# Performance work log

Hardware: AMD Instinct MI355X
Metric: run time of the kernel (lower is better)

The kernel has to match this reference:

```python
import jax, jax.numpy as jnp
import numpy as np

B, D, L, H, W, T = 256, 512, 32, 14, 14, 8


def _lin(x, w, b=None):
    y = x @ w.T
    return y if b is None else y + b


def _conv1x1(x, w, b):  # x: [B,C,H,W], w: [O,C], b: [O]
    return jnp.einsum('oc,bchw->bohw', w, x) + b[None, :, None, None]


def setup_inputs() -> dict:
    key = jax.random.key(0)
    ks = jax.random.split(key, 24)
    s = 0.02
    inp = {
        'c': jax.random.normal(ks[0], (B, D), jnp.float32),
        'm': jax.random.normal(ks[1], (B, D), jnp.float32),
        'k': jax.random.normal(ks[2], (B, D, H, W), jnp.float32),
        'q': jax.random.normal(ks[3], (B, D), jnp.float32),
        'cw': jax.random.normal(ks[4], (B, L, D), jnp.float32),
        'mask': jax.random.randint(ks[5], (B, L), 0, 2, jnp.int32),
        'cs': jax.random.normal(ks[6], (T, B, D), jnp.float32),
        'ms': jax.random.normal(ks[7], (T, B, D), jnp.float32),
        # ControlUnit params
        'Wcq': jax.random.normal(ks[8], (D, 2 * D), jnp.float32) * s,
        'bcq': jnp.zeros((D,), jnp.float32),
        'Wca': jax.random.normal(ks[9], (1, D), jnp.float32) * s,
        'bca': jnp.zeros((1,), jnp.float32),
        # ReadUnit params
        'Wm_r': jax.random.normal(ks[10], (D, D), jnp.float32) * s,
        'bm_r': jnp.zeros((D,), jnp.float32),
        'Wk': jax.random.normal(ks[11], (D, D), jnp.float32) * s,
        'bk': jnp.zeros((D,), jnp.float32),
        'WI': jax.random.normal(ks[12], (D, 2 * D), jnp.float32) * s,
        'bI': jnp.zeros((D,), jnp.float32),
        'Wra': jax.random.normal(ks[13], (D, D), jnp.float32) * s,
        'bra': jnp.zeros((D,), jnp.float32),
        # WriteUnit params
        'Wm_w': jax.random.normal(ks[14], (D, 2 * D), jnp.float32) * s,
        'bm_w': jnp.zeros((D,), jnp.float32),
        'Wsa': jax.random.normal(ks[15], (1, D), jnp.float32) * s,
        'bsa': jnp.zeros((1,), jnp.float32),
        'Wm2': jax.random.normal(ks[16], (D, D), jnp.float32) * s,
        'bm2': jnp.zeros((D,), jnp.float32),
        'Wc': jax.random.normal(ks[17], (1, D), jnp.float32) * s,
        'bc': jnp.ones((1,), jnp.float32),  # linear_c.bias.data.fill_(1)
        'Ws': jax.random.normal(ks[18], (D, D), jnp.float32) * s,
    }
    return inp


def reference(c, m, k, q, cw, mask, cs, ms,
              Wcq, bcq, Wca, bca,
              Wm_r, bm_r, Wk, bk, WI, bI, Wra, bra,
              Wm_w, bm_w, Wsa, bsa, Wm2, bm2, Wc, bc, Ws):
    # ---- ControlUnit ----
    cq = _lin(jnp.concatenate([c, q], axis=1), Wcq, bcq)          # [B,D]
    ca = _lin(cq[:, None, :] * cw, Wca, bca)                      # [B,L,1]
    ca = jnp.where(mask[:, :, None] > 0, ca, -jnp.inf)            # mask padding
    cv = jax.nn.softmax(ca, axis=1)                               # [B,L,1]
    c_new = jnp.sum(cv * cw, axis=1)                              # [B,D]

    # ---- ReadUnit ----
    mI = _lin(m, Wm_r, bm_r)                                      # [B,D]
    I = mI[:, :, None, None] * _conv1x1(k, Wk, bk)                # [B,D,H,W]
    I_ = _conv1x1(jnp.concatenate([I, k], axis=1), WI, bI)        # [B,D,H,W]
    ra = _conv1x1(I_ * c_new[:, :, None, None], Wra, bra)         # [B,D,H,W]
    rv = jax.nn.softmax(ra, axis=1)                               # Softmax2d = over channels
    r = jnp.sum(rv * k, axis=(-1, -2))                            # [B,D]

    # ---- WriteUnit ----
    m_prev = _lin(jnp.concatenate([r, m], axis=1), Wm_w, bm_w)    # [B,D]
    m_ = _lin(m_prev, Wm2, bm2)                                   # [B,D]
    gate = jax.nn.sigmoid(_lin(c_new, Wc, bc))                    # [B,1]
    sa = jax.nn.softmax(_lin(cs * gate[None, :, :], Wsa, bsa), axis=0)  # [T,B,1]
    m_sa = jnp.sum(sa * ms, axis=0)                               # [B,D]
    m_ = m_ + m_sa @ Ws.T
    m_new = gate * m + (1.0 - gate) * m_                          # [B,D]

    return (c_new, m_new, cv, rv)
```

## Files before the change

### kernel.cpp

```cpp
#include <hip/hip_runtime.h>
#include <hip/hip_bf16.h>

#define BB 256
#define DD 512
#define LL 32
#define HWN 196
#define TT 8

typedef __hip_bfloat16 bf16;
typedef __attribute__((ext_vector_type(8))) short short8;
typedef __attribute__((ext_vector_type(4))) float f32x4;

__device__ __forceinline__ float b2f(bf16 x) { return __bfloat162float(x); }
__device__ __forceinline__ bf16 f2b(float x) { return __float2bfloat16(x); }
__device__ __forceinline__ unsigned short f2bu(float x) {
    bf16 h = __float2bfloat16(x);
    return *(unsigned short*)&h;
}
#define NEG_INF (-__builtin_huge_valf())

__global__ __launch_bounds__(256) void cvt_w_kernel(
    const float* __restrict__ src, unsigned short* __restrict__ dst, int n4)
{
    int i = blockIdx.x*256 + threadIdx.x;
    if (i < n4) {
        float4 f = ((const float4*)src)[i];
        ushort4 u;
        u.x = f2bu(f.x); u.y = f2bu(f.y); u.z = f2bu(f.z); u.w = f2bu(f.w);
        ((ushort4*)dst)[i] = u;
    }
}

__global__ __launch_bounds__(256) void small_gemm_kernel(
    const float* __restrict__ A1, int K1,
    const float* __restrict__ A2, int K2,
    const float* __restrict__ Wt, const float* __restrict__ bias,
    float* __restrict__ outf, int Dout)
{
    __shared__ float xs[1024];
    int b = blockIdx.x, tid = threadIdx.x;
    int K = K1 + K2;
    for (int i = tid; i < K; i += 256) {
        xs[i] = (i < K1) ? A1[(size_t)b*K1 + i] : A2[(size_t)b*K2 + (i - K1)];
    }
    __syncthreads();
    for (int d = tid; d < Dout; d += 256) {
        const float4* wrow = (const float4*)(Wt + (size_t)d * K);
        float acc = 0.f;
        for (int j = 0; j < K/4; ++j) {
            float4 w = wrow[j];
            acc += w.x*xs[j*4] + w.y*xs[j*4+1] + w.z*xs[j*4+2] + w.w*xs[j*4+3];
        }
        if (bias) acc += bias[d];
        outf[(size_t)b*Dout + d] = acc;
    }
}

__global__ __launch_bounds__(256) void control_kernel(
    const float* __restrict__ cq, const float* __restrict__ cw,
    const float* __restrict__ Wca, const float* __restrict__ bca,
    const int* __restrict__ mask,
    float* __restrict__ cnew_f, float* __restrict__ cv_out, float* __restrict__ cnew_out)
{
    __shared__ float u[DD];
    __shared__ float cas[LL];
    __shared__ float cvs[LL];
    int b = blockIdx.x, tid = threadIdx.x;
    for (int d = tid; d < DD; d += 256) u[d] = cq[(size_t)b*DD + d] * Wca[d];
    __syncthreads();
    int wave = tid >> 6, lane = tid & 63;
    float bca0 = bca[0];
    for (int lw = 0; lw < 8; ++lw) {
        int l = wave*8 + lw;
        const float4* w4 = (const float4*)(cw + ((size_t)(b*LL + l))*DD + lane*8);
        float4 wa = w4[0], wb = w4[1];
        const float* uu = &u[lane*8];
        float p = wa.x*uu[0] + wa.y*uu[1] + wa.z*uu[2] + wa.w*uu[3]
                + wb.x*uu[4] + wb.y*uu[5] + wb.z*uu[6] + wb.w*uu[7];
        for (int off = 32; off > 0; off >>= 1) p += __shfl_down(p, off);
        if (lane == 0) {
            float v = p + bca0;
            if (mask[b*LL + l] <= 0) v = NEG_INF;
            cas[l] = v;
        }
    }
    __syncthreads();
    if (tid < LL) {
        float mx = NEG_INF;
        for (int j = 0; j < LL; ++j) mx = fmaxf(mx, cas[j]);
        float s = 0.f;
        for (int j = 0; j < LL; ++j) s += __expf(cas[j] - mx);
        float cv = __expf(cas[tid] - mx) / s;
        cvs[tid] = cv;
        cv_out[b*LL + tid] = cv;
    }
    __syncthreads();
    for (int d = tid; d < DD; d += 256) {
        float acc = 0.f;
        for (int l = 0; l < LL; ++l) acc += cvs[l] * cw[((size_t)(b*LL + l))*DD + d];
        cnew_f[(size_t)b*DD + d] = acc;
        cnew_out[(size_t)b*DD + d] = acc;
    }
}

__device__ __forceinline__ void load4rows(const void* X, int isf32, size_t row, int n4, ushort4 r[4]) {
    if (isf32) {
        const float* p = (const float*)X + row*HWN + n4*4;
        #pragma unroll
        for (int i = 0; i < 4; ++i) {
            float4 f = *(const float4*)(p + (size_t)i*HWN);
            r[i].x = f2bu(f.x); r[i].y = f2bu(f.y); r[i].z = f2bu(f.z); r[i].w = f2bu(f.w);
        }
    } else {
        const unsigned short* p = (const unsigned short*)X + row*HWN + n4*4;
        #pragma unroll
        for (int i = 0; i < 4; ++i) r[i] = *(const ushort4*)(p + (size_t)i*HWN);
    }
}

__global__ __launch_bounds__(512) void conv_mfma_kernel(
    const void* __restrict__ X1, int x1f32, int C1,
    const void* __restrict__ X2, int x2f32,
    const unsigned short* __restrict__ Wb, int C,
    const float* __restrict__ bias, const float* __restrict__ oscale,
    unsigned short* __restrict__ Y)
{
    __shared__ __align__(16) uint2 Xs[8*212];
    int b = blockIdx.x, ot = blockIdx.y;
    int tid = threadIdx.x;
    int wave = tid >> 6, lane = tid & 63;
    int wm = wave >> 1, wn = wave & 1;
    int obase = ot*128 + wm*32;
    int n0 = wn*112;
    int ntn = wn ? 6 : 7;
    int ln = lane & 15, lq = lane >> 4;
    int C2 = C - C1;

    int n4_0 = tid % 49, kq_0 = tid / 49;
    bool st = tid < 8*49;

    f32x4 acc[2][7];
    #pragma unroll
    for (int mt = 0; mt < 2; ++mt)
        #pragma unroll
        for (int nt = 0; nt < 7; ++nt) acc[mt][nt] = (f32x4){0.f, 0.f, 0.f, 0.f};

    for (int c0 = 0; c0 < C; c0 += 32) {
        __syncthreads();
        if (st) {
            int c = c0 + kq_0*4;
            ushort4 r[4];
            if (c < C1) load4rows(X1, x1f32, (size_t)b*C1 + c, n4_0, r);
            else        load4rows(X2, x2f32, (size_t)b*C2 + (c - C1), n4_0, r);
            uint2* cell = &Xs[kq_0*212 + n4_0*4];
            *(uint4*)(cell) = make_uint4(
                (uint)r[0].x | ((uint)r[1].x << 16), (uint)r[2].x | ((uint)r[3].x << 16),
                (uint)r[0].y | ((uint)r[1].y << 16), (uint)r[2].y | ((uint)r[3].y << 16));
            *(uint4*)(cell + 2) = make_uint4(
                (uint)r[0].z | ((uint)r[1].z << 16), (uint)r[2].z | ((uint)r[3].z << 16),
                (uint)r[0].w | ((uint)r[1].w << 16), (uint)r[2].w | ((uint)r[3].w << 16));
        }
        __syncthreads();
        short8 a[2];
        #pragma unroll
        for (int mt = 0; mt < 2; ++mt)
            a[mt] = *(const short8*)(Wb + (size_t)(obase + mt*16 + ln)*C + c0 + lq*8);
        #pragma unroll
        for (int nt = 0; nt < 7; ++nt) {
            if (nt < ntn) {
                int n = n0 + nt*16 + ln;
                uint2 b0 = Xs[(lq*2)*212 + n];
                uint2 b1 = Xs[(lq*2 + 1)*212 + n];
                union { uint4 u; short8 s8; } bb;
                bb.u = make_uint4(b0.x, b0.y, b1.x, b1.y);
                #pragma unroll
                for (int mt = 0; mt < 2; ++mt)
                    acc[mt][nt] = __builtin_amdgcn_mfma_f32_16x16x32_bf16(a[mt], bb.s8, acc[mt][nt], 0, 0, 0);
            }
        }
    }
    #pragma unroll
    for (int mt = 0; mt < 2; ++mt) {
        #pragma unroll
        for (int rr = 0; rr < 4; ++rr) {
            int o = obase + mt*16 + lq*4 + rr;
            float bo = bias[o];
            float os = oscale ? oscale[(size_t)b*DD + o] : 1.f;
            #pragma unroll
            for (int nt = 0; nt < 7; ++nt) {
                int hw = n0 + nt*16 + ln;
                if (nt < ntn && hw < HWN) {
                    float v = (acc[mt][nt][rr] + bo) * os;
                    Y[((size_t)b*DD + o)*HWN + hw] = f2bu(v);
                }
            }
        }
    }
}

__global__ __launch_bounds__(512) void softmax_r_kernel(
    const bf16* __restrict__ ra, const float* __restrict__ kin,
    float* __restrict__ rv, float* __restrict__ r)
{
    __shared__ float pm[2][HWN], ps[2][HWN];
    __shared__ float mxs[HWN], sis[HWN];
    int b = blockIdx.x, tid = threadIdx.x;
    int half = tid >> 8, hw = tid & 255;
    if (hw < HWN) {
        float m = NEG_INF, s = 0.f;
        const bf16* base = ra + ((size_t)b*DD + half*256)*HWN + hw;
        for (int c = 0; c < 256; ++c) {
            float x = b2f(base[(size_t)c*HWN]);
            float nm = fmaxf(m, x);
            s = s*__expf(m - nm) + __expf(x - nm);
            m = nm;
        }
        pm[half][hw] = m; ps[half][hw] = s;
    }
    __syncthreads();
    if (tid < HWN) {
        float m0 = pm[0][tid], m1 = pm[1][tid];
        float m = fmaxf(m0, m1);
        float s = ps[0][tid]*__expf(m0 - m) + ps[1][tid]*__expf(m1 - m);
        mxs[tid] = m; sis[tid] = 1.f/s;
    }
    __syncthreads();
    int wave = tid >> 6, lane = tid & 63;
    for (int ci = 0; ci < 64; ++ci) {
        int c = wave*64 + ci;
        float psum = 0.f;
        #pragma unroll
        for (int g = 0; g < 4; ++g) {
            int hw2 = lane + 64*g;
            if (hw2 < HWN) {
                size_t idx = ((size_t)b*DD + c)*HWN + hw2;
                float e = __expf(b2f(ra[idx]) - mxs[hw2]) * sis[hw2];
                rv[idx] = e;
                psum += e * kin[idx];
            }
        }
        for (int off = 32; off > 0; off >>= 1) psum += __shfl_down(psum, off);
        if (lane == 0) r[(size_t)b*DD + c] = psum;
    }
}

__global__ __launch_bounds__(256) void samsa_kernel(
    const float* __restrict__ cs, const float* __restrict__ ms,
    const float* __restrict__ Wsa, const float* __restrict__ bsa,
    const float* __restrict__ cnew, const float* __restrict__ Wc, const float* __restrict__ bc,
    float* __restrict__ gate_out, float* __restrict__ msa)
{
    __shared__ float lg[TT];
    __shared__ float sas[TT];
    __shared__ float xw[DD];
    __shared__ float gsh;
    int b = blockIdx.x, tid = threadIdx.x;
    int wave = tid >> 6, lane = tid & 63;
    for (int d = tid; d < DD; d += 256) xw[d] = Wsa[d];
    __syncthreads();
    for (int tw = 0; tw < 2; ++tw) {
        int t = wave + 4*tw;
        const float4* c4 = (const float4*)(cs + ((size_t)t*BB + b)*DD + lane*8);
        float4 ca = c4[0], cb = c4[1];
        const float* ww = &xw[lane*8];
        float p = ca.x*ww[0] + ca.y*ww[1] + ca.z*ww[2] + ca.w*ww[3]
                + cb.x*ww[4] + cb.y*ww[5] + cb.z*ww[6] + cb.w*ww[7];
        for (int off = 32; off > 0; off >>= 1) p += __shfl_down(p, off);
        if (lane == 0) lg[t] = p;
    }
    if (wave == 0) {
        const float4* w4 = (const float4*)(Wc + lane*8);
        const float* x = &cnew[(size_t)b*DD + lane*8];
        float4 wa = w4[0], wb = w4[1];
        float p = wa.x*x[0] + wa.y*x[1] + wa.z*x[2] + wa.w*x[3]
                + wb.x*x[4] + wb.y*x[5] + wb.z*x[6] + wb.w*x[7];
        for (int off = 32; off > 0; off >>= 1) p += __shfl_down(p, off);
        if (lane == 0) {
            float g = 1.f / (1.f + __expf(-(p + bc[0])));
            gsh = g; gate_out[b] = g;
        }
    }
    __syncthreads();
    if (tid < TT) {
        float g = gsh, b0 = bsa[0];
        float mx = NEG_INF;
        for (int j = 0; j < TT; ++j) mx = fmaxf(mx, g*lg[j] + b0);
        float s = 0.f;
        for (int j = 0; j < TT; ++j) s += __expf(g*lg[j] + b0 - mx);
        sas[tid] = __expf(g*lg[tid] + b0 - mx) / s;
    }
    __syncthreads();
    for (int d = tid; d < DD; d += 256) {
        float acc = 0.f;
        for (int t = 0; t < TT; ++t) acc += sas[t] * ms[((size_t)t*BB + b)*DD + d];
        msa[(size_t)b*DD + d] = acc;
    }
}

__global__ __launch_bounds__(256) void write_final_kernel(
    const float* __restrict__ msa, const float* __restrict__ Ws,
    const float* __restrict__ m, const float* __restrict__ gate,
    const float* __restrict__ mund, float* __restrict__ mnew)
{
    __shared__ float xs[DD];
    int b = blockIdx.x, tid = threadIdx.x;
    for (int i = tid; i < DD; i += 256) xs[i] = msa[(size_t)b*DD + i];
    __syncthreads();
    float g = gate[b];
    for (int d = tid; d < DD; d += 256) {
        const float4* wrow = (const float4*)(Ws + (size_t)d * DD);
        float acc = 0.f;
        for (int j = 0; j < DD/4; ++j) {
            float4 w = wrow[j];
            acc += w.x*xs[j*4] + w.y*xs[j*4+1] + w.z*xs[j*4+2] + w.w*xs[j*4+3];
        }
        size_t idx = (size_t)b*DD + d;
        mnew[idx] = g * m[idx] + (1.f - g) * (mund[idx] + acc);
    }
}

extern "C" void kernel_launch(void* const* d_in, const int* in_sizes, int n_in,
                              void* d_out, int out_size, void* d_ws, size_t ws_size,
                              hipStream_t stream)
{
    (void)in_sizes; (void)n_in; (void)out_size; (void)ws_size;
    const float* c    = (const float*)d_in[0];
    const float* m    = (const float*)d_in[1];
    const float* k    = (const float*)d_in[2];
    const float* q    = (const float*)d_in[3];
    const float* cw   = (const float*)d_in[4];
    const int*   mask = (const int*)  d_in[5];
    const float* cs   = (const float*)d_in[6];
    const float* ms   = (const float*)d_in[7];
    const float* Wcq  = (const float*)d_in[8];
    const float* bcq  = (const float*)d_in[9];
    const float* Wca  = (const float*)d_in[10];
    const float* bca  = (const float*)d_in[11];
    const float* Wm_r = (const float*)d_in[12];
    const float* bm_r = (const float*)d_in[13];
    const float* Wk   = (const float*)d_in[14];
    const float* bk   = (const float*)d_in[15];
    const float* WI   = (const float*)d_in[16];
    const float* bI   = (const float*)d_in[17];
    const float* Wra  = (const float*)d_in[18];
    const float* bra  = (const float*)d_in[19];
    const float* Wm_w = (const float*)d_in[20];
    const float* bm_w = (const float*)d_in[21];
    const float* Wsa  = (const float*)d_in[22];
    const float* bsa  = (const float*)d_in[23];
    const float* Wm2  = (const float*)d_in[24];
    const float* bm2  = (const float*)d_in[25];
    const float* Wc   = (const float*)d_in[26];
    const float* bc   = (const float*)d_in[27];
    const float* Ws   = (const float*)d_in[28];

    float* out_cnew = (float*)d_out;
    float* out_mnew = out_cnew + BB*DD;
    float* out_cv   = out_mnew + BB*DD;
    float* out_rv   = out_cv + BB*LL;

    unsigned short* I_w  = (unsigned short*)out_rv;
    unsigned short* I2_w = (unsigned short*)((char*)out_rv + 51380224);

    char* w = (char*)d_ws;
    float* s0      = (float*)(w + 0);
    float* s1      = (float*)(w + 524288);
    float* s2      = (float*)(w + 1048576);
    float* s3      = (float*)(w + 1572864);
    unsigned short* Wkb  = (unsigned short*)(w + 2097152);
    unsigned short* WIb  = (unsigned short*)(w + 2621440);
    unsigned short* Wrab = (unsigned short*)(w + 3670016);
    unsigned short* ra_w = (unsigned short*)(w + 4194304);
    float* gate_w  = (float*)(w + 55574528);

    float* cq_w   = s0;
    float* r_w    = s0;
    float* cnew_w = s1;
    float* mI_w   = s2;
    float* mund_w = s2;
    float* mprev_w= s3;
    float* msa_w  = s3;

    cvt_w_kernel<<<256, 256, 0, stream>>>(Wk,  Wkb,  65536);
    cvt_w_kernel<<<512, 256, 0, stream>>>(WI,  WIb,  131072);
    cvt_w_kernel<<<256, 256, 0, stream>>>(Wra, Wrab, 65536);

    small_gemm_kernel<<<BB, 256, 0, stream>>>(c, DD, q, DD, Wcq, bcq, cq_w, DD);
    small_gemm_kernel<<<BB, 256, 0, stream>>>(m, DD, nullptr, 0, Wm_r, bm_r, mI_w, DD);
    control_kernel<<<BB, 256, 0, stream>>>(cq_w, cw, Wca, bca, mask, cnew_w, out_cv, out_cnew);

    conv_mfma_kernel<<<dim3(BB, 4), 512, 0, stream>>>(k,    1, DD, nullptr, 0, Wkb,  DD,   bk,  mI_w,   I_w);
    conv_mfma_kernel<<<dim3(BB, 4), 512, 0, stream>>>(I_w,  0, DD, k,       1, WIb,  2*DD, bI,  cnew_w, I2_w);
    conv_mfma_kernel<<<dim3(BB, 4), 512, 0, stream>>>(I2_w, 0, DD, nullptr, 0, Wrab, DD,   bra, nullptr, ra_w);
    softmax_r_kernel<<<BB, 512, 0, stream>>>((const bf16*)ra_w, k, out_rv, r_w);

    small_gemm_kernel<<<BB, 256, 0, stream>>>(r_w, DD, m, DD, Wm_w, bm_w, mprev_w, DD);
    small_gemm_kernel<<<BB, 256, 0, stream>>>(mprev_w, DD, nullptr, 0, Wm2, bm2, mund_w, DD);
    samsa_kernel<<<BB, 256, 0, stream>>>(cs, ms, Wsa, bsa, cnew_w, Wc, bc, gate_w, msa_w);
    write_final_kernel<<<BB, 256, 0, stream>>>(msa_w, Ws, m, gate_w, mund_w, out_mnew);
}
```

Measured before the change: 776.1 us.

## Pre-pack conv inputs into MFMA-ready bf16 tiles and double-buffer LDS via direct loads

Adds a pack kernel that converts k into bf16 chunks already laid out the way the MFMA B-operand expects, and makes the first two conv kernels write their outputs in that packed layout. The conv kernel now stages each 32-channel step with global_load_lds straight into a double-buffered LDS tile, prefetching the next step while computing the current one, and drops the per-thread conversion and shuffling during staging. This removes one barrier per step and overlaps loads with MFMA. The cost is an extra pack pass over k, twice the LDS use, and workspace aliasing, since the packed k shares its buffer with ra.

```diff
diff --git a/kernel.cpp b/kernel.cpp
--- a/kernel.cpp
+++ b/kernel.cpp
@@ -6,18 +6,29 @@
 #define LL 32
 #define HWN 196
 #define TT 8
+#define STEPB 12544
 
 typedef __hip_bfloat16 bf16;
 typedef __attribute__((ext_vector_type(8))) short short8;
 typedef __attribute__((ext_vector_type(4))) float f32x4;
 
 __device__ __forceinline__ float b2f(bf16 x) { return __bfloat162float(x); }
-__device__ __forceinline__ bf16 f2b(float x) { return __float2bfloat16(x); }
 __device__ __forceinline__ unsigned short f2bu(float x) {
     bf16 h = __float2bfloat16(x);
     return *(unsigned short*)&h;
 }
 #define NEG_INF (-__builtin_huge_valf())
+
+__device__ __forceinline__ void gload_lds16(const void* g, void* l) {
+    __builtin_amdgcn_global_load_lds(
+        (const __attribute__((address_space(1))) void*)g,
+        (__attribute__((address_space(3))) void*)l, 16, 0, 0);
+}
+__device__ __forceinline__ void gload_lds4(const void* g, void* l) {
+    __builtin_amdgcn_global_load_lds(
+        (const __attribute__((address_space(1))) void*)g,
+        (__attribute__((address_space(3))) void*)l, 4, 0, 0);
+}
 
 __global__ __launch_bounds__(256) void cvt_w_kernel(
     const float* __restrict__ src, unsigned short* __restrict__ dst, int n4)
@@ -28,6 +39,30 @@
         ushort4 u;
         u.x = f2bu(f.x); u.y = f2bu(f.y); u.z = f2bu(f.z); u.w = f2bu(f.w);
         ((ushort4*)dst)[i] = u;
+    }
+}
+
+__global__ __launch_bounds__(256) void pack_x_kernel(
+    const float* __restrict__ X, char* __restrict__ Xp)
+{
+    int b = blockIdx.x, s = blockIdx.y;
+    uint2* chunk = (uint2*)(Xp + ((size_t)(b*16 + s))*STEPB);
+    for (int idx = threadIdx.x; idx < 8*49; idx += 256) {
+        int kq = idx / 49, n4 = idx % 49;
+        const float* p = X + ((size_t)b*DD + s*32 + kq*4)*HWN + n4*4;
+        ushort4 r[4];
+        #pragma unroll
+        for (int i = 0; i < 4; ++i) {
+            float4 f = *(const float4*)(p + (size_t)i*HWN);
+            r[i].x = f2bu(f.x); r[i].y = f2bu(f.y); r[i].z = f2bu(f.z); r[i].w = f2bu(f.w);
+        }
+        uint2* cell = chunk + kq*196 + n4*4;
+        *(uint4*)(cell) = make_uint4(
+            (uint)r[0].x | ((uint)r[1].x << 16), (uint)r[2].x | ((uint)r[3].x << 16),
+            (uint)r[0].y | ((uint)r[1].y << 16), (uint)r[2].y | ((uint)r[3].y << 16));
+        *(uint4*)(cell + 2) = make_uint4(
+            (uint)r[0].z | ((uint)r[1].z << 16), (uint)r[2].z | ((uint)r[3].z << 16),
+            (uint)r[0].w | ((uint)r[1].w << 16), (uint)r[2].w | ((uint)r[3].w << 16));
     }
 }
 
@@ -103,29 +138,14 @@
     }
 }
 
-__device__ __forceinline__ void load4rows(const void* X, int isf32, size_t row, int n4, ushort4 r[4]) {
-    if (isf32) {
-        const float* p = (const float*)X + row*HWN + n4*4;
-        #pragma unroll
-        for (int i = 0; i < 4; ++i) {
-            float4 f = *(const float4*)(p + (size_t)i*HWN);
-            r[i].x = f2bu(f.x); r[i].y = f2bu(f.y); r[i].z = f2bu(f.z); r[i].w = f2bu(f.w);
-        }
-    } else {
-        const unsigned short* p = (const unsigned short*)X + row*HWN + n4*4;
-        #pragma unroll
-        for (int i = 0; i < 4; ++i) r[i] = *(const ushort4*)(p + (size_t)i*HWN);
-    }
-}
-
 __global__ __launch_bounds__(512) void conv_mfma_kernel(
-    const void* __restrict__ X1, int x1f32, int C1,
-    const void* __restrict__ X2, int x2f32,
+    const char* __restrict__ X1p, int ns1,
+    const char* __restrict__ X2p, int ns2,
     const unsigned short* __restrict__ Wb, int C,
     const float* __restrict__ bias, const float* __restrict__ oscale,
-    unsigned short* __restrict__ Y)
-{
-    __shared__ __align__(16) uint2 Xs[8*212];
+    void* __restrict__ Yout, int packed_out)
+{
+    __shared__ __align__(16) char Xs[2][12800];
     int b = blockIdx.x, ot = blockIdx.y;
     int tid = threadIdx.x;
     int wave = tid >> 6, lane = tid & 63;
@@ -134,10 +154,15 @@
     int n0 = wn*112;
     int ntn = wn ? 6 : 7;
     int ln = lane & 15, lq = lane >> 4;
-    int C2 = C - C1;
-
-    int n4_0 = tid % 49, kq_0 = tid / 49;
-    bool st = tid < 8*49;
+
+    auto STAGE = [&](int s, char* lb) {
+        const char* chunk = (s < ns1) ? X1p + ((size_t)b*ns1 + s)*STEPB
+                                      : X2p + ((size_t)b*ns2 + (s - ns1))*STEPB;
+        for (int i = wave; i < 13; i += 8) {
+            if (i < 12) gload_lds16(chunk + i*1024 + lane*16, lb + i*1024);
+            else        gload_lds4 (chunk + 12288 + lane*4,  lb + 12288);
+        }
+    };
 
     f32x4 acc[2][7];
     #pragma unroll
@@ -145,53 +170,72 @@
         #pragma unroll
         for (int nt = 0; nt < 7; ++nt) acc[mt][nt] = (f32x4){0.f, 0.f, 0.f, 0.f};
 
-    for (int c0 = 0; c0 < C; c0 += 32) {
+    STAGE(0, Xs[0]);
+    int nsteps = ns1 + ns2;
+    for (int s = 0; s < nsteps; ++s) {
+        char* cur = Xs[s & 1];
+        char* nxt = Xs[(s & 1) ^ 1];
         __syncthreads();
-        if (st) {
-            int c = c0 + kq_0*4;
-            ushort4 r[4];
-            if (c < C1) load4rows(X1, x1f32, (size_t)b*C1 + c, n4_0, r);
-            else        load4rows(X2, x2f32, (size_t)b*C2 + (c - C1), n4_0, r);
-            uint2* cell = &Xs[kq_0*212 + n4_0*4];
-            *(uint4*)(cell) = make_uint4(
-                (uint)r[0].x | ((uint)r[1].x << 16), (uint)r[2].x | ((uint)r[3].x << 16),
-                (uint)r[0].y | ((uint)r[1].y << 16), (uint)r[2].y | ((uint)r[3].y << 16));
-            *(uint4*)(cell + 2) = make_uint4(
-                (uint)r[0].z | ((uint)r[1].z << 16), (uint)r[2].z | ((uint)r[3].z << 16),
-                (uint)r[0].w | ((uint)r[1].w << 16), (uint)r[2].w | ((uint)r[3].w << 16));
-        }
-        __syncthreads();
-        short8 a[2];
-        #pragma unroll
-        for (int mt = 0; mt < 2; ++mt)
-            a[mt] = *(const short8*)(Wb + (size_t)(obase + mt*16 + ln)*C + c0 + lq*8);
+        short8 a0 = *(const short8*)(Wb + (size_t)(obase + ln)*C + s*32 + lq*8);
+        short8 a1 = *(const short8*)(Wb + (size_t)(obase + 16 + ln)*C + s*32 + lq*8);
+        __builtin_amdgcn_sched_barrier(0);
+        if (s + 1 < nsteps) STAGE(s + 1, nxt);
+        const uint2* cells = (const uint2*)cur;
         #pragma unroll
         for (int nt = 0; nt < 7; ++nt) {
             if (nt < ntn) {
                 int n = n0 + nt*16 + ln;
-                uint2 b0 = Xs[(lq*2)*212 + n];
-                uint2 b1 = Xs[(lq*2 + 1)*212 + n];
+                uint2 c0 = cells[(lq*2)*196 + n];
+                uint2 c1 = cells[(lq*2 + 1)*196 + n];
                 union { uint4 u; short8 s8; } bb;
-                bb.u = make_uint4(b0.x, b0.y, b1.x, b1.y);
-                #pragma unroll
-                for (int mt = 0; mt < 2; ++mt)
-                    acc[mt][nt] = __builtin_amdgcn_mfma_f32_16x16x32_bf16(a[mt], bb.s8, acc[mt][nt], 0, 0, 0);
+                bb.u = make_uint4(c0.x, c0.y, c1.x, c1.y);
+                acc[0][nt] = __builtin_amdgcn_mfma_f32_16x16x32_bf16(a0, bb.s8, acc[0][nt], 0, 0, 0);
+                acc[1][nt] = __builtin_amdgcn_mfma_f32_16x16x32_bf16(a1, bb.s8, acc[1][nt], 0, 0, 0);
             }
         }
     }
-    #pragma unroll
-    for (int mt = 0; mt < 2; ++mt) {
-        #pragma unroll
-        for (int rr = 0; rr < 4; ++rr) {
-            int o = obase + mt*16 + lq*4 + rr;
-            float bo = bias[o];
-            float os = oscale ? oscale[(size_t)b*DD + o] : 1.f;
+    if (packed_out) {
+        uint2* Yp = (uint2*)Yout;
+        #pragma unroll
+        for (int mt = 0; mt < 2; ++mt) {
+            int o4 = obase + mt*16 + lq*4;
+            int st = o4 >> 5, kqo = (o4 & 31) >> 2;
+            float bo[4], os[4];
+            #pragma unroll
+            for (int rr = 0; rr < 4; ++rr) {
+                bo[rr] = bias[o4 + rr];
+                os[rr] = oscale ? oscale[(size_t)b*DD + o4 + rr] : 1.f;
+            }
             #pragma unroll
             for (int nt = 0; nt < 7; ++nt) {
                 int hw = n0 + nt*16 + ln;
                 if (nt < ntn && hw < HWN) {
-                    float v = (acc[mt][nt][rr] + bo) * os;
-                    Y[((size_t)b*DD + o)*HWN + hw] = f2bu(v);
+                    unsigned short v[4];
+                    #pragma unroll
+                    for (int rr = 0; rr < 4; ++rr)
+                        v[rr] = f2bu((acc[mt][nt][rr] + bo[rr]) * os[rr]);
+                    Yp[((size_t)(b*16 + st)*8 + kqo)*196 + hw] =
+                        make_uint2((uint)v[0] | ((uint)v[1] << 16),
+                                   (uint)v[2] | ((uint)v[3] << 16));
+                }
+            }
+        }
+    } else {
+        unsigned short* Y = (unsigned short*)Yout;
+        #pragma unroll
+        for (int mt = 0; mt < 2; ++mt) {
+            #pragma unroll
+            for (int rr = 0; rr < 4; ++rr) {
+                int o = obase + mt*16 + lq*4 + rr;
+                float bo = bias[o];
+                float os = oscale ? oscale[(size_t)b*DD + o] : 1.f;
+                #pragma unroll
+                for (int nt = 0; nt < 7; ++nt) {
+                    int hw = n0 + nt*16 + ln;
+                    if (nt < ntn && hw < HWN) {
+                        float v = (acc[mt][nt][rr] + bo) * os;
+                        Y[((size_t)b*DD + o)*HWN + hw] = f2bu(v);
+                    }
                 }
             }
         }
@@ -359,8 +403,8 @@
     float* out_cv   = out_mnew + BB*DD;
     float* out_rv   = out_cv + BB*LL;
 
-    unsigned short* I_w  = (unsigned short*)out_rv;
-    unsigned short* I2_w = (unsigned short*)((char*)out_rv + 51380224);
+    char* Ip  = (char*)out_rv;
+    char* I2p = (char*)out_rv + 51380224;
 
     char* w = (char*)d_ws;
     float* s0      = (float*)(w + 0);
@@ -370,7 +414,7 @@
     unsigned short* Wkb  = (unsigned short*)(w + 2097152);
     unsigned short* WIb  = (unsigned short*)(w + 2621440);
     unsigned short* Wrab = (unsigned short*)(w + 3670016);
-    unsigned short* ra_w = (unsigned short*)(w + 4194304);
+    char* kp_ra = (char*)(w + 4194304);
     float* gate_w  = (float*)(w + 55574528);
 
     float* cq_w   = s0;
@@ -380,18 +424,21 @@
     float* mund_w = s2;
     float* mprev_w= s3;
     float* msa_w  = s3;
+    unsigned short* ra_w = (unsigned short*)kp_ra;
 
     cvt_w_kernel<<<256, 256, 0, stream>>>(Wk,  Wkb,  65536);
     cvt_w_kernel<<<512, 256, 0, stream>>>(WI,  WIb,  131072);
     cvt_w_kernel<<<256, 256, 0, stream>>>(Wra, Wrab, 65536);
 
+    pack_x_kernel<<<dim3(BB, 16), 256, 0, stream>>>(k, kp_ra);
+
     small_gemm_kernel<<<BB, 256, 0, stream>>>(c, DD, q, DD, Wcq, bcq, cq_w, DD);
     small_gemm_kernel<<<BB, 256, 0, stream>>>(m, DD, nullptr, 0, Wm_r, bm_r, mI_w, DD);
     control_kernel<<<BB, 256, 0, stream>>>(cq_w, cw, Wca, bca, mask, cnew_w, out_cv, out_cnew);
 
-    conv_mfma_kernel<<<dim3(BB, 4), 512, 0, stream>>>(k,    1, DD, nullptr, 0, Wkb,  DD,   bk,  mI_w,   I_w);
-    conv_mfma_kernel<<<dim3(BB, 4), 512, 0, stream>>>(I_w,  0, DD, k,       1, WIb,  2*DD, bI,  cnew_w, I2_w);
-    conv_mfma_kernel<<<dim3(BB, 4), 512, 0, stream>>>(I2_w, 0, DD, nullptr, 0, Wrab, DD,   bra, nullptr, ra_w);
+    conv_mfma_kernel<<<dim3(BB, 4), 512, 0, stream>>>(kp_ra, 16, nullptr, 0,  Wkb,  DD,   bk,  mI_w,   Ip,   1);
+    conv_mfma_kernel<<<dim3(BB, 4), 512, 0, stream>>>(Ip,    16, kp_ra,  16,  WIb,  2*DD, bI,  cnew_w, I2p,  1);
+    conv_mfma_kernel<<<dim3(BB, 4), 512, 0, stream>>>(I2p,   16, nullptr, 0,  Wrab, DD,   bra, nullptr, ra_w, 0);
     softmax_r_kernel<<<BB, 512, 0, stream>>>((const bf16*)ra_w, k, out_rv, r_w);
 
     small_gemm_kernel<<<BB, 256, 0, stream>>>(r_w, DD, m, DD, Wm_w, bm_w, mprev_w, DD);
```

After: 791.8 us. 2.0% more time.
